# Kernel tuning notes

Measured on AMD Instinct MI355X. Metric: run time of the kernel, lower is better.

## Reference

```python
import jax, jax.numpy as jnp
import numpy as np

EPS = 1e-5

def _layernorm(x, w, b):
    mu = jnp.mean(x, axis=-1, keepdims=True)
    var = jnp.mean(jnp.square(x - mu), axis=-1, keepdims=True)
    return (x - mu) * jax.lax.rsqrt(var + EPS) * w + b

def setup_inputs() -> dict:
    key = jax.random.key(0)
    ks = jax.random.split(key, 8)
    B, P, N, T = 64, 3, 512, 1024
    Tmax = 25
    xs = jax.random.normal(ks[0], (B, P, N, T), dtype=jnp.float32)
    init_h = jnp.zeros((B, N), dtype=jnp.float32)
    # Affine gate params: init_gamma=0.1, init_beta=1 (perturbed slightly for generality)
    gamma = 0.1 + 0.01 * jax.random.normal(ks[1], (P, N), dtype=jnp.float32)
    beta = jnp.ones((P, N), dtype=jnp.float32) + 0.01 * jax.random.normal(ks[2], (P, N), dtype=jnp.float32)
    # Integrator h2h: Linear(N, 2N, bias=False) + LayerNorm(2N) (weight=0.1, bias=0)
    Wh2h = jax.random.normal(ks[3], (2 * N, N), dtype=jnp.float32) / np.sqrt(N)
    lnh_w = jnp.full((2 * N,), 0.1, dtype=jnp.float32)
    lnh_b = jnp.zeros((2 * N,), dtype=jnp.float32)
    # Integrator x2h: Linear(N, N, bias=False) + LayerNorm(N) (weight=0.1, bias=-log U(1,Tmax-1))
    Wx2h = jax.random.normal(ks[4], (N, N), dtype=jnp.float32) / np.sqrt(N)
    lnx_w = jnp.full((N,), 0.1, dtype=jnp.float32)
    lnx_b = -jnp.log(jax.random.uniform(ks[5], (N,), minval=1.0, maxval=float(Tmax - 1), dtype=jnp.float32))
    return {"xs": xs, "init_h": init_h, "gamma": gamma, "beta": beta,
            "Wh2h": Wh2h, "lnh_w": lnh_w, "lnh_b": lnh_b,
            "Wx2h": Wx2h, "lnx_w": lnx_w, "lnx_b": lnx_b}

def reference(xs, init_h, gamma, beta, Wh2h, lnh_w, lnh_b, Wx2h, lnx_w, lnx_b):
    # xs: [B, P, N, T]; init_h: [B, N]
    N = init_h.shape[-1]

    def step(h, xx_t):
        # xx_t: [B, P, N]. Pathway gating (Layer): Affine(hx) -> sigmoid -> gate inputs
        g_path = jax.nn.sigmoid(gamma * h[:, None, :] + beta)          # [B, P, N]
        in_layer = jax.nn.relu(jnp.sum(g_path * xx_t, axis=1))          # [B, N]
        # Integrator
        hh = _layernorm(h @ Wh2h.T, lnh_w, lnh_b)                       # [B, 2N]
        h_i, h_g = hh[:, :N], hh[:, N:]
        x = jax.nn.relu(in_layer + h_i)                                 # [B, N]
        gg = jax.nn.sigmoid(_layernorm(x @ Wx2h.T, lnx_w, lnx_b) + h_g)
        h_new = (1.0 - gg) * h + gg * x
        return h_new, h_new

    xs_t = jnp.transpose(xs, (3, 0, 1, 2))                              # [T, B, P, N]
    _, h_all = jax.lax.scan(step, init_h, xs_t)                         # [T, B, N]
    return jnp.transpose(h_all, (1, 2, 0))                              # [B, N, T]
```

## Files before the change

kernel.cpp:

```cpp
#include <hip/hip_runtime.h>

#define EPSF 1e-5f

typedef unsigned short u16;
typedef unsigned int u32;

__device__ __forceinline__ u16 f2bf(float f) {
  u32 u = __float_as_uint(f);
  u += 0x7fffu + ((u >> 16) & 1u);
  return (u16)(u >> 16);
}
__device__ __forceinline__ u32 packbf(float lo, float hi) {
  return (u32)f2bf(lo) | ((u32)f2bf(hi) << 16);
}

#if __has_builtin(__builtin_amdgcn_fdot2_f32_bf16)
typedef __attribute__((ext_vector_type(2))) __bf16 bf16x2;
__device__ __forceinline__ float dot2bf(u32 w, u32 h, float acc) {
  union { u32 u; bf16x2 v; } a, b; a.u = w; b.u = h;
  return __builtin_amdgcn_fdot2_f32_bf16(a.v, b.v, acc, false);
}
#else
__device__ __forceinline__ float dot2bf(u32 w, u32 h, float acc) {
  float r = fmaf(__uint_as_float(w << 16), __uint_as_float(h << 16), acc);
  return fmaf(__uint_as_float(w & 0xffff0000u), __uint_as_float(h & 0xffff0000u), r);
}
#endif

__global__ void prep_weights(const float* __restrict__ W1, const float* __restrict__ W2,
                             u16* __restrict__ W1p, u16* __restrict__ W2p) {
  int i = blockIdx.x * blockDim.x + threadIdx.x;
  if (i < 1024 * 64) {
    int j = i >> 6, kk = i & 63;
    const float* src = W1 + (size_t)j * 512 + kk * 8;
    u16* dst = W1p + ((size_t)(kk * 1024 + j)) * 8;
    #pragma unroll
    for (int r = 0; r < 8; ++r) dst[r] = f2bf(src[r]);
  }
  if (i < 512 * 64) {
    int n = i >> 6, kk = i & 63;
    const float* src = W2 + (size_t)n * 512 + kk * 8;
    u16* dst = W2p + ((size_t)(kk * 512 + n)) * 8;
    #pragma unroll
    for (int r = 0; r < 8; ++r) dst[r] = f2bf(src[r]);
  }
}

__global__ __launch_bounds__(1024)
void rnn_kernel(const float* __restrict__ xs, const float* __restrict__ h0,
                const float* __restrict__ gamma, const float* __restrict__ beta,
                const u16* __restrict__ W1p,
                const float* __restrict__ lnh_w, const float* __restrict__ lnh_b,
                const u16* __restrict__ W2p,
                const float* __restrict__ lnx_w, const float* __restrict__ lnx_b,
                float* __restrict__ out) {
  const int b = blockIdx.x;
  const int tid = threadIdx.x;
  const int N = 512;

  __shared__ float hg_s[512];
  __shared__ float p2[1024];
  __shared__ u32 hb2[256];
  __shared__ u32 xb2[256];
  __shared__ float red_s[16], red_q[16];
  __shared__ float stat[4];
  __shared__ __align__(16) float out_t[32][512];
  __shared__ float pad_[2560];

  const int w = tid >> 6;

  const float w1w = lnh_w[tid], w1b = lnh_b[tid];
  float g0 = 0, g1 = 0, g2 = 0, b0 = 0, b1 = 0, b2 = 0, w2w = 0, w2b = 0;
  float hv = 0.f, xv = 0.f, il = 0.f;
  if (tid < N) {
    g0 = gamma[0 * N + tid]; g1 = gamma[1 * N + tid]; g2 = gamma[2 * N + tid];
    b0 = beta[0 * N + tid];  b1 = beta[1 * N + tid];  b2 = beta[2 * N + tid];
    w2w = lnx_w[tid]; w2b = lnx_b[tid];
    hv = h0[(size_t)b * N + tid];
    float hnb = __shfl_down(hv, 1);
    if (!(tid & 1)) hb2[tid >> 1] = packbf(hv, hnb);
  }
  if (gamma[0] > 1e30f) pad_[0] = 1.f;
  const float* xs_b = xs + (size_t)b * 3 * N * 1024;
  __syncthreads();

  for (int t0 = 0; t0 < 1024; t0 += 4) {
    float4 xr0, xr1, xr2;
    if (tid < N) {
      xr0 = *(const float4*)(xs_b + (size_t)(0 * N + tid) * 1024 + t0);
      xr1 = *(const float4*)(xs_b + (size_t)(1 * N + tid) * 1024 + t0);
      xr2 = *(const float4*)(xs_b + (size_t)(2 * N + tid) * 1024 + t0);
    }
    #pragma unroll
    for (int q = 0; q < 4; ++q) {
      const int t = t0 + q;
      const int tt = t & 31;

      if (tid < N) {
        float s0 = 1.f / (1.f + __expf(-(g0 * hv + b0)));
        float s1 = 1.f / (1.f + __expf(-(g1 * hv + b1)));
        float s2 = 1.f / (1.f + __expf(-(g2 * hv + b2)));
        float x0 = (q == 0) ? xr0.x : (q == 1) ? xr0.y : (q == 2) ? xr0.z : xr0.w;
        float x1 = (q == 0) ? xr1.x : (q == 1) ? xr1.y : (q == 2) ? xr1.z : xr1.w;
        float x2 = (q == 0) ? xr2.x : (q == 1) ? xr2.y : (q == 2) ? xr2.z : xr2.w;
        il = fmaxf(s0 * x0 + s1 * x1 + s2 * x2, 0.f);
      }

      float acc;
      {
        const u32* wp = (const u32*)W1p + (size_t)tid * 4;
        float a0 = 0.f, a1 = 0.f;
        #pragma unroll 8
        for (int kk = 0; kk < 64; ++kk) {
          uint4 wv = *(const uint4*)(wp + (size_t)kk * 4096);
          uint4 hv4 = *(const uint4*)(hb2 + kk * 4);
          a0 = dot2bf(wv.x, hv4.x, a0); a1 = dot2bf(wv.y, hv4.y, a1);
          a0 = dot2bf(wv.z, hv4.z, a0); a1 = dot2bf(wv.w, hv4.w, a1);
        }
        acc = a0 + a1;
      }

      {
        float s = acc, qq = acc * acc;
        #pragma unroll
        for (int off = 32; off > 0; off >>= 1) {
          s += __shfl_down(s, off); qq += __shfl_down(qq, off);
        }
        if ((tid & 63) == 0) { red_s[w] = s; red_q[w] = qq; }
      }
      __syncthreads();
      if (tid == 0) {
        float ss = 0.f, qq = 0.f;
        #pragma unroll
        for (int i = 0; i < 16; ++i) { ss += red_s[i]; qq += red_q[i]; }
        float mu = ss * (1.f / 1024.f);
        float var = qq * (1.f / 1024.f) - mu * mu;
        stat[0] = mu; stat[1] = rsqrtf(var + EPSF);
      }
      __syncthreads();

      {
        float hh = (acc - stat[0]) * stat[1] * w1w + w1b;
        if (tid < N) {
          xv = fmaxf(il + hh, 0.f);
          float xnb = __shfl_down(xv, 1);
          if (!(tid & 1)) xb2[tid >> 1] = packbf(xv, xnb);
        } else {
          hg_s[tid - N] = hh;
        }
      }
      __syncthreads();

      {
        const int n = tid & 511;
        const int half = tid >> 9;
        const u32* wp = (const u32*)W2p + (size_t)n * 4 + (size_t)(half * 32) * 2048;
        const u32* xp = xb2 + half * 128;
        float c0 = 0.f, c1 = 0.f;
        #pragma unroll 8
        for (int kk = 0; kk < 32; ++kk) {
          uint4 wv = *(const uint4*)(wp + (size_t)kk * 2048);
          uint4 xv4 = *(const uint4*)(xp + kk * 4);
          c0 = dot2bf(wv.x, xv4.x, c0); c1 = dot2bf(wv.y, xv4.y, c1);
          c0 = dot2bf(wv.z, xv4.z, c0); c1 = dot2bf(wv.w, xv4.w, c1);
        }
        p2[tid] = c0 + c1;
      }
      __syncthreads();

      float accf = 0.f;
      {
        float s = 0.f, qq = 0.f;
        if (tid < N) {
          accf = p2[tid] + p2[tid + 512];
          s = accf; qq = accf * accf;
        }
        #pragma unroll
        for (int off = 32; off > 0; off >>= 1) {
          s += __shfl_down(s, off); qq += __shfl_down(qq, off);
        }
        if ((tid & 63) == 0) { red_s[w] = s; red_q[w] = qq; }
      }
      __syncthreads();
      if (tid == 0) {
        float ss = 0.f, qq = 0.f;
        #pragma unroll
        for (int i = 0; i < 16; ++i) { ss += red_s[i]; qq += red_q[i]; }
        float mu = ss * (1.f / 512.f);
        float var = qq * (1.f / 512.f) - mu * mu;
        stat[2] = mu; stat[3] = rsqrtf(var + EPSF);
      }
      __syncthreads();

      if (tid < N) {
        float y = (accf - stat[2]) * stat[3] * w2w + w2b;
        float gg = 1.f / (1.f + __expf(-(y + hg_s[tid])));
        float hn = hv + gg * (xv - hv);
        out_t[tt][tid] = hn;
        hv = hn;
        float hnb = __shfl_down(hn, 1);
        if (!(tid & 1)) hb2[tid >> 1] = packbf(hn, hnb);
      }
      __syncthreads();

      if (tt == 31) {
        const int n = tid >> 1;
        const int seg = tid & 1;
        float* op = out + ((size_t)b * N + n) * 1024 + (t - 31) + seg * 16;
        #pragma unroll
        for (int i = 0; i < 4; ++i) {
          float4 v;
          v.x = out_t[seg * 16 + i * 4 + 0][n];
          v.y = out_t[seg * 16 + i * 4 + 1][n];
          v.z = out_t[seg * 16 + i * 4 + 2][n];
          v.w = out_t[seg * 16 + i * 4 + 3][n];
          *(float4*)(op + i * 4) = v;
        }
      }
    }
  }
}

extern "C" void kernel_launch(void* const* d_in, const int* in_sizes, int n_in,
                              void* d_out, int out_size, void* d_ws, size_t ws_size,
                              hipStream_t stream) {
  const float* xs    = (const float*)d_in[0];
  const float* h0    = (const float*)d_in[1];
  const float* gamma = (const float*)d_in[2];
  const float* beta  = (const float*)d_in[3];
  const float* W1    = (const float*)d_in[4];
  const float* lnh_w = (const float*)d_in[5];
  const float* lnh_b = (const float*)d_in[6];
  const float* W2    = (const float*)d_in[7];
  const float* lnx_w = (const float*)d_in[8];
  const float* lnx_b = (const float*)d_in[9];
  float* out = (float*)d_out;

  u16* W1p = (u16*)d_ws;
  u16* W2p = W1p + (size_t)1024 * 512;

  prep_weights<<<(65536 + 255) / 256, 256, 0, stream>>>(W1, W2, W1p, W2p);
  rnn_kernel<<<64, 1024, 0, stream>>>(xs, h0, gamma, beta, W1p,
                                      lnh_w, lnh_b, W2p, lnx_w, lnx_b, out);
}
```

Baseline: 17.78 ms.

## Replace single-thread LayerNorm stats with redundant per-thread reductions; prefetch weights in batches

The tid==0 serial reduction and its extra barrier per LayerNorm are removed. Every thread now reads the 16 wave partials and reduces them with xor shuffles, which cuts two block barriers per timestep. The weight-streaming matvec loops are restructured to prefetch 8 uint4 weight vectors ahead into registers with four accumulators, raising memory-level parallelism. The shared-memory padding array, which had limited occupancy, is dropped. The cost is higher register pressure from the 16-entry uint4 buffers.

```diff
diff --git a/kernel.cpp b/kernel.cpp
--- a/kernel.cpp
+++ b/kernel.cpp
@@ -63,9 +63,7 @@
   __shared__ u32 hb2[256];
   __shared__ u32 xb2[256];
   __shared__ float red_s[16], red_q[16];
-  __shared__ float stat[4];
   __shared__ __align__(16) float out_t[32][512];
-  __shared__ float pad_[2560];
 
   const int w = tid >> 6;
 
@@ -80,8 +78,10 @@
     float hnb = __shfl_down(hv, 1);
     if (!(tid & 1)) hb2[tid >> 1] = packbf(hv, hnb);
   }
-  if (gamma[0] > 1e30f) pad_[0] = 1.f;
   const float* xs_b = xs + (size_t)b * 3 * N * 1024;
+  const uint4* w1 = ((const uint4*)W1p) + tid;
+  const int n2 = tid & 511, half = tid >> 9;
+  const uint4* w2 = ((const uint4*)W2p) + n2 + (size_t)half * 32 * 512;
   __syncthreads();
 
   for (int t0 = 0; t0 < 1024; t0 += 4) {
@@ -96,28 +96,40 @@
       const int t = t0 + q;
       const int tt = t & 31;
 
-      if (tid < N) {
-        float s0 = 1.f / (1.f + __expf(-(g0 * hv + b0)));
-        float s1 = 1.f / (1.f + __expf(-(g1 * hv + b1)));
-        float s2 = 1.f / (1.f + __expf(-(g2 * hv + b2)));
-        float x0 = (q == 0) ? xr0.x : (q == 1) ? xr0.y : (q == 2) ? xr0.z : xr0.w;
-        float x1 = (q == 0) ? xr1.x : (q == 1) ? xr1.y : (q == 2) ? xr1.z : xr1.w;
-        float x2 = (q == 0) ? xr2.x : (q == 1) ? xr2.y : (q == 2) ? xr2.z : xr2.w;
-        il = fmaxf(s0 * x0 + s1 * x1 + s2 * x2, 0.f);
-      }
-
       float acc;
       {
-        const u32* wp = (const u32*)W1p + (size_t)tid * 4;
-        float a0 = 0.f, a1 = 0.f;
-        #pragma unroll 8
-        for (int kk = 0; kk < 64; ++kk) {
-          uint4 wv = *(const uint4*)(wp + (size_t)kk * 4096);
-          uint4 hv4 = *(const uint4*)(hb2 + kk * 4);
-          a0 = dot2bf(wv.x, hv4.x, a0); a1 = dot2bf(wv.y, hv4.y, a1);
-          a0 = dot2bf(wv.z, hv4.z, a0); a1 = dot2bf(wv.w, hv4.w, a1);
-        }
-        acc = a0 + a1;
+        const uint4* hp = (const uint4*)hb2;
+        uint4 wv[8];
+        #pragma unroll
+        for (int u = 0; u < 8; ++u) wv[u] = w1[u * 1024];
+
+        if (tid < N) {
+          float s0 = 1.f / (1.f + __expf(-(g0 * hv + b0)));
+          float s1 = 1.f / (1.f + __expf(-(g1 * hv + b1)));
+          float s2 = 1.f / (1.f + __expf(-(g2 * hv + b2)));
+          float x0 = (q == 0) ? xr0.x : (q == 1) ? xr0.y : (q == 2) ? xr0.z : xr0.w;
+          float x1 = (q == 0) ? xr1.x : (q == 1) ? xr1.y : (q == 2) ? xr1.z : xr1.w;
+          float x2 = (q == 0) ? xr2.x : (q == 1) ? xr2.y : (q == 2) ? xr2.z : xr2.w;
+          il = fmaxf(s0 * x0 + s1 * x1 + s2 * x2, 0.f);
+        }
+
+        float a0 = 0.f, a1 = 0.f, a2 = 0.f, a3 = 0.f;
+        #pragma unroll
+        for (int c = 0; c < 8; ++c) {
+          uint4 nx[8];
+          #pragma unroll
+          for (int u = 0; u < 8; ++u)
+            if (c < 7) nx[u] = w1[((c + 1) * 8 + u) * 1024];
+          #pragma unroll
+          for (int u = 0; u < 8; ++u) {
+            uint4 hv4 = hp[c * 8 + u];
+            a0 = dot2bf(wv[u].x, hv4.x, a0); a1 = dot2bf(wv[u].y, hv4.y, a1);
+            a2 = dot2bf(wv[u].z, hv4.z, a2); a3 = dot2bf(wv[u].w, hv4.w, a3);
+          }
+          #pragma unroll
+          for (int u = 0; u < 8; ++u) wv[u] = nx[u];
+        }
+        acc = (a0 + a1) + (a2 + a3);
       }
 
       {
@@ -129,18 +141,20 @@
         if ((tid & 63) == 0) { red_s[w] = s; red_q[w] = qq; }
       }
       __syncthreads();
-      if (tid == 0) {
-        float ss = 0.f, qq = 0.f;
-        #pragma unroll
-        for (int i = 0; i < 16; ++i) { ss += red_s[i]; qq += red_q[i]; }
-        float mu = ss * (1.f / 1024.f);
+      float mu, rinv;
+      {
+        float s = red_s[tid & 15], qq = red_q[tid & 15];
+        #pragma unroll
+        for (int off = 8; off > 0; off >>= 1) {
+          s += __shfl_xor(s, off); qq += __shfl_xor(qq, off);
+        }
+        mu = s * (1.f / 1024.f);
         float var = qq * (1.f / 1024.f) - mu * mu;
-        stat[0] = mu; stat[1] = rsqrtf(var + EPSF);
-      }
-      __syncthreads();
-
-      {
-        float hh = (acc - stat[0]) * stat[1] * w1w + w1b;
+        rinv = rsqrtf(var + EPSF);
+      }
+
+      {
+        float hh = (acc - mu) * rinv * w1w + w1b;
         if (tid < N) {
           xv = fmaxf(il + hh, 0.f);
           float xnb = __shfl_down(xv, 1);
@@ -152,19 +166,27 @@
       __syncthreads();
 
       {
-        const int n = tid & 511;
-        const int half = tid >> 9;
-        const u32* wp = (const u32*)W2p + (size_t)n * 4 + (size_t)(half * 32) * 2048;
-        const u32* xp = xb2 + half * 128;
-        float c0 = 0.f, c1 = 0.f;
-        #pragma unroll 8
-        for (int kk = 0; kk < 32; ++kk) {
-          uint4 wv = *(const uint4*)(wp + (size_t)kk * 2048);
-          uint4 xv4 = *(const uint4*)(xp + kk * 4);
-          c0 = dot2bf(wv.x, xv4.x, c0); c1 = dot2bf(wv.y, xv4.y, c1);
-          c0 = dot2bf(wv.z, xv4.z, c0); c1 = dot2bf(wv.w, xv4.w, c1);
-        }
-        p2[tid] = c0 + c1;
+        const uint4* xp = ((const uint4*)xb2) + half * 32;
+        uint4 wv[8];
+        #pragma unroll
+        for (int u = 0; u < 8; ++u) wv[u] = w2[u * 512];
+        float c0 = 0.f, c1 = 0.f, c2 = 0.f, c3 = 0.f;
+        #pragma unroll
+        for (int c = 0; c < 4; ++c) {
+          uint4 nx[8];
+          #pragma unroll
+          for (int u = 0; u < 8; ++u)
+            if (c < 3) nx[u] = w2[((c + 1) * 8 + u) * 512];
+          #pragma unroll
+          for (int u = 0; u < 8; ++u) {
+            uint4 xv4 = xp[c * 8 + u];
+            c0 = dot2bf(wv[u].x, xv4.x, c0); c1 = dot2bf(wv[u].y, xv4.y, c1);
+            c2 = dot2bf(wv[u].z, xv4.z, c2); c3 = dot2bf(wv[u].w, xv4.w, c3);
+          }
+          #pragma unroll
+          for (int u = 0; u < 8; ++u) wv[u] = nx[u];
+        }
+        p2[tid] = (c0 + c1) + (c2 + c3);
       }
       __syncthreads();
 
@@ -182,24 +204,25 @@
         if ((tid & 63) == 0) { red_s[w] = s; red_q[w] = qq; }
       }
       __syncthreads();
-      if (tid == 0) {
-        float ss = 0.f, qq = 0.f;
-        #pragma unroll
-        for (int i = 0; i < 16; ++i) { ss += red_s[i]; qq += red_q[i]; }
-        float mu = ss * (1.f / 512.f);
-        float var = qq * (1.f / 512.f) - mu * mu;
-        stat[2] = mu; stat[3] = rsqrtf(var + EPSF);
-      }
-      __syncthreads();
-
-      if (tid < N) {
-        float y = (accf - stat[2]) * stat[3] * w2w + w2b;
-        float gg = 1.f / (1.f + __expf(-(y + hg_s[tid])));
-        float hn = hv + gg * (xv - hv);
-        out_t[tt][tid] = hn;
-        hv = hn;
-        float hnb = __shfl_down(hn, 1);
-        if (!(tid & 1)) hb2[tid >> 1] = packbf(hn, hnb);
+      {
+        float s = red_s[tid & 15], qq = red_q[tid & 15];
+        #pragma unroll
+        for (int off = 8; off > 0; off >>= 1) {
+          s += __shfl_xor(s, off); qq += __shfl_xor(qq, off);
+        }
+        float mu2 = s * (1.f / 512.f);
+        float var2 = qq * (1.f / 512.f) - mu2 * mu2;
+        float rinv2 = rsqrtf(var2 + EPSF);
+
+        if (tid < N) {
+          float y = (accf - mu2) * rinv2 * w2w + w2b;
+          float gg = 1.f / (1.f + __expf(-(y + hg_s[tid])));
+          float hn = hv + gg * (xv - hv);
+          out_t[tt][tid] = hn;
+          hv = hn;
+          float hnb = __shfl_down(hn, 1);
+          if (!(tid & 1)) hb2[tid >> 1] = packbf(hn, hnb);
+        }
       }
       __syncthreads();
 
```

After: 39.98 ms. 2.25x slower.
